# Kernel tuning notes

Hardware: AMD Instinct MI355X
Metric: run time of the kernel (lower is better)

Reference implementation:

```python
import jax, jax.numpy as jnp
import numpy as np

WS, SS, NH = 7, 3, 16  # window_size, shift_size, num_heads


def _rel_pos_index(ws):
    coords = np.stack(np.meshgrid(np.arange(ws), np.arange(ws), indexing='ij'))  # (2, ws, ws)
    cf = coords.reshape(2, -1)                       # (2, N)
    rel = (cf[:, :, None] - cf[:, None, :]).transpose(1, 2, 0).copy()  # (N, N, 2)
    rel[:, :, 0] += ws - 1
    rel[:, :, 1] += ws - 1
    rel[:, :, 0] *= 2 * ws - 1
    return rel.sum(-1)                               # (N, N) int indices into bias table


def _attn_mask(Hp, Wp, ws, ss):
    img = np.zeros((Hp, Wp))
    slices = (slice(0, -ws), slice(-ws, -ss), slice(-ss, None))
    cnt = 0
    for h in slices:
        for w in slices:
            img[h, w] = cnt
            cnt += 1
    mw = img.reshape(Hp // ws, ws, Wp // ws, ws).transpose(0, 2, 1, 3).reshape(-1, ws * ws)  # (nW, N)
    am = mw[:, None, :] - mw[:, :, None]             # (nW, N, N)
    return np.where(am != 0, -100.0, 0.0).astype(np.float32)


def setup_inputs() -> dict:
    key = jax.random.key(0)
    k1, k2, k3, k4 = jax.random.split(key, 4)
    B, H, W, C = 16, 56, 56, 512
    return {
        'q_out': jax.random.normal(k1, (B, H, W, C), dtype=jnp.float32),
        'k_out': jax.random.normal(k2, (B, H, W, C), dtype=jnp.float32),
        'v_out': jax.random.normal(k3, (B, H, W, C), dtype=jnp.float32),
        'bias_table': 0.02 * jax.random.normal(k4, ((2 * WS - 1) ** 2, NH), dtype=jnp.float32),
        'C': C, 'H': H, 'W': W,
        'x_low_padding_h': 0, 'x_low_padding_w': 0,
    }


def reference(q_out, k_out, v_out, bias_table, C, H, W, x_low_padding_h, x_low_padding_w):
    ws, ss, nh = WS, SS, NH
    Hp, Wp = H + x_low_padding_h, W + x_low_padding_w
    B = q_out.shape[0]
    hd = C // nh
    scale = hd ** (-0.5)
    N = ws * ws

    def part(x):  # (B,Hp,Wp,C) -> (B*nW, N, C)
        x = x.reshape(B, Hp // ws, ws, Wp // ws, ws, C).transpose(0, 1, 3, 2, 4, 5)
        return x.reshape(-1, N, C)

    # cyclic shift
    sq = jnp.roll(q_out, (-ss, -ss), axis=(1, 2))
    sk = jnp.roll(k_out, (-ss, -ss), axis=(1, 2))
    sv = jnp.roll(v_out, (-ss, -ss), axis=(1, 2))

    qw, kw, vw = part(sq), part(sk), part(sv)
    B_ = qw.shape[0]
    q = qw.reshape(B_, N, nh, hd).transpose(0, 2, 1, 3) * scale  # (B_, nh, N, hd)
    k = kw.reshape(B_, N, nh, hd).transpose(0, 2, 1, 3)
    v = vw.reshape(B_, N, nh, hd).transpose(0, 2, 1, 3)

    attn = jnp.einsum('bhnd,bhmd->bhnm', q, k)  # (B_, nh, N, N)

    # relative position bias
    rpi = _rel_pos_index(ws)
    bias = bias_table[rpi.reshape(-1)].reshape(N, N, nh).transpose(2, 0, 1)  # (nh, N, N)
    attn = attn + bias[None]

    # shift mask
    am = jnp.asarray(_attn_mask(Hp, Wp, ws, ss), dtype=attn.dtype)  # (nW, N, N)
    nW = am.shape[0]
    attn = attn.reshape(B_ // nW, nW, nh, N, N) + am[None, :, None]
    attn = jax.nn.softmax(attn.reshape(B_, nh, N, N), axis=-1)

    xw = jnp.einsum('bhnm,bhmd->bhnd', attn, v).transpose(0, 2, 1, 3).reshape(B_, N, C)

    # window reverse + reverse shift
    x = xw.reshape(B, Hp // ws, Wp // ws, ws, ws, C).transpose(0, 1, 3, 2, 4, 5).reshape(B, Hp, Wp, C)
    return jnp.roll(x, (ss, ss), axis=(1, 2))
```

## Files before the change

### kernel.cpp

```cpp
#include <hip/hip_runtime.h>
#include <stdint.h>


constexpr int WSZ  = 7;
constexpr int NTOK = 49;
constexpr int NH_  = 16;
constexpr int HD_  = 32;
constexpr int SP   = 56;
constexpr int CH   = 512;
constexpr float LOG2E = 1.4426950408889634f;

typedef float  f32x4 __attribute__((ext_vector_type(4)));
typedef short  s16x8 __attribute__((ext_vector_type(8)));

union FragU { uint32_t w[4]; s16x8 v; };

__device__ inline uint32_t bf16_hibits(float x) {
    uint32_t u = __float_as_uint(x);
    u += 0x7fffu + ((u >> 16) & 1u);
    return u & 0xffff0000u;
}

__device__ inline uint32_t pk_bf16(float a, float b) {
    return (bf16_hibits(a) >> 16) | bf16_hibits(b);
}

__device__ inline void hilo_pair(float a, float b, uint32_t& wh, uint32_t& wl) {
    uint32_t ah = bf16_hibits(a), bh = bf16_hibits(b);
    wh = (ah >> 16) | bh;
    float ra = a - __uint_as_float(ah);
    float rb = b - __uint_as_float(bh);
    wl = pk_bf16(ra, rb);
}

__global__ __launch_bounds__(256)
void build_bm(const float* __restrict__ bias, float* __restrict__ bm)
{
    const int blk = blockIdx.x;
    const int h = blk >> 2, cls = blk & 3;
    for (int idx = threadIdx.x; idx < 4096; idx += 256) {
        const int q = idx >> 6, m = idx & 63;
        float val;
        if (q >= NTOK || m >= NTOK) {
            val = -1e9f;
        } else {
            const int iq = q / 7, jq = q % 7, im = m / 7, jm = m % 7;
            const int rpi = (iq - im + 6) * 13 + (jq - jm + 6);
            const float bv = bias[rpi * NH_ + h];
            const int rq = ((cls & 2) ? (iq < 4 ? 3 : 6) : 0)
                         + ((cls & 1) ? (jq < 4 ? 1 : 2) : 0);
            const int rm = ((cls & 2) ? (im < 4 ? 3 : 6) : 0)
                         + ((cls & 1) ? (jm < 4 ? 1 : 2) : 0);
            const float mask = (rq != rm) ? -100.0f : 0.0f;
            val = (bv + mask) * LOG2E - 23.0f;
        }
        bm[blk * 4096 + idx] = val;
    }
}

__global__ __launch_bounds__(256, 2)
void swin_mfma_kernel(const float* __restrict__ qg,
                      const float* __restrict__ kg,
                      const float* __restrict__ vg,
                      const float* __restrict__ bm,
                      float* __restrict__ outg)
{
    const int wave = threadIdx.x >> 6;
    const int wh   = blockIdx.x * 4 + wave;
    const int h    = wh & (NH_ - 1);
    const int w    = wh >> 4;
    const int wc   = w & 7;
    const int wr   = (w >> 3) & 7;
    const int b    = w >> 6;

    const int lane = threadIdx.x & 63;
    const int g    = lane >> 4;
    const int l16  = lane & 15;

    const int t  = lane < NTOK ? lane : NTOK - 1;
    const int it = t / 7, jt = t - 7 * it;
    int sr = wr * 7 + it + 3; if (sr >= SP) sr -= SP;
    int sc = wc * 7 + jt + 3; if (sc >= SP) sc -= SP;
    const int off_t = ((b * SP + sr) * SP + sc) * CH + h * HD_;

    const float qs = 0.17677669529663687f * LOG2E;

    float4 qa[4][2], ka[4][2];
#pragma unroll
    for (int tt = 0; tt < 4; ++tt) {
        const int o = __shfl(off_t, 16 * tt + l16);
        const float* qp = qg + o + 8 * g;
        const float* kp = kg + o + 8 * g;
        qa[tt][0] = *(const float4*)qp;
        qa[tt][1] = *(const float4*)(qp + 4);
        ka[tt][0] = *(const float4*)kp;
        ka[tt][1] = *(const float4*)(kp + 4);
    }

    float vr[2][2][8];
#pragma unroll
    for (int mc = 0; mc < 2; ++mc)
#pragma unroll
        for (int e = 0; e < 8; ++e) {
            const int o = __shfl(off_t, 32 * mc + 8 * g + e);
#pragma unroll
            for (int dh = 0; dh < 2; ++dh)
                vr[mc][dh][e] = vg[o + 16 * dh + l16];
        }

    s16x8 Qh[4], Ql[4], Kh[4], Kl[4];
#pragma unroll
    for (int tt = 0; tt < 4; ++tt) {
        FragU qh, ql, kh, kl;
        float qf[8] = { qa[tt][0].x * qs, qa[tt][0].y * qs, qa[tt][0].z * qs, qa[tt][0].w * qs,
                        qa[tt][1].x * qs, qa[tt][1].y * qs, qa[tt][1].z * qs, qa[tt][1].w * qs };
        float kf[8] = { ka[tt][0].x, ka[tt][0].y, ka[tt][0].z, ka[tt][0].w,
                        ka[tt][1].x, ka[tt][1].y, ka[tt][1].z, ka[tt][1].w };
#pragma unroll
        for (int wd = 0; wd < 4; ++wd) {
            hilo_pair(qf[2 * wd], qf[2 * wd + 1], qh.w[wd], ql.w[wd]);
            hilo_pair(kf[2 * wd], kf[2 * wd + 1], kh.w[wd], kl.w[wd]);
        }
        Qh[tt] = qh.v; Ql[tt] = ql.v; Kh[tt] = kh.v; Kl[tt] = kl.v;
    }

    const int cls = ((wr == 7) ? 2 : 0) | ((wc == 7) ? 1 : 0);
    const float* bmh = bm + (h * 4 + cls) * 4096;

    f32x4 accS[4][4];
#pragma unroll
    for (int tq = 0; tq < 4; ++tq)
#pragma unroll
        for (int tk = 0; tk < 4; ++tk)
            accS[tq][tk] = *(const f32x4*)(bmh + (16 * tq + l16) * 64 + 16 * tk + 4 * g);

#pragma unroll
    for (int tq = 0; tq < 4; ++tq)
#pragma unroll
        for (int tk = 0; tk < 4; ++tk) {
            f32x4 a = accS[tq][tk];
            a = __builtin_amdgcn_mfma_f32_16x16x32_bf16(Kl[tk], Qh[tq], a, 0, 0, 0);
            a = __builtin_amdgcn_mfma_f32_16x16x32_bf16(Kh[tk], Ql[tq], a, 0, 0, 0);
            a = __builtin_amdgcn_mfma_f32_16x16x32_bf16(Kh[tk], Qh[tq], a, 0, 0, 0);
            accS[tq][tk] = a;
        }

    float p[4][4][4];
    float inv[4];
#pragma unroll
    for (int tq = 0; tq < 4; ++tq) {
        float d0 = 0.f, d1 = 0.f, d2 = 0.f, d3 = 0.f;
#pragma unroll
        for (int tk = 0; tk < 4; ++tk) {
            float e0 = __builtin_amdgcn_exp2f(accS[tq][tk][0]);
            float e1 = __builtin_amdgcn_exp2f(accS[tq][tk][1]);
            float e2 = __builtin_amdgcn_exp2f(accS[tq][tk][2]);
            float e3 = __builtin_amdgcn_exp2f(accS[tq][tk][3]);
            p[tq][tk][0] = e0; p[tq][tk][1] = e1;
            p[tq][tk][2] = e2; p[tq][tk][3] = e3;
            d0 += e0; d1 += e1; d2 += e2; d3 += e3;
        }
        float ds = (d0 + d1) + (d2 + d3);
        ds += __shfl_xor(ds, 16);
        ds += __shfl_xor(ds, 32);
        inv[tq] = 1.0f / (ds + 1e-30f);
    }

    uint32_t u0[4][4], u1[4][4];
#pragma unroll
    for (int tq = 0; tq < 4; ++tq)
#pragma unroll
        for (int tk = 0; tk < 4; ++tk) {
            u0[tq][tk] = pk_bf16(p[tq][tk][0], p[tq][tk][1]);
            u1[tq][tk] = pk_bf16(p[tq][tk][2], p[tq][tk][3]);
        }

    const int srcb = 32 * (g & 1) + l16;
    const bool hiG = (lane >= 32);
    s16x8 PA[4][2];
#pragma unroll
    for (int tq = 0; tq < 4; ++tq)
#pragma unroll
        for (int mc = 0; mc < 2; ++mc) {
            FragU fu;
#pragma unroll
            for (int wd = 0; wd < 4; ++wd) {
                const int sl = srcb + 16 * (wd >> 1);
                uint32_t A, B;
                if (wd & 1) {
                    A = __shfl(u1[tq][2 * mc],     sl);
                    B = __shfl(u1[tq][2 * mc + 1], sl);
                } else {
                    A = __shfl(u0[tq][2 * mc],     sl);
                    B = __shfl(u0[tq][2 * mc + 1], sl);
                }
                fu.w[wd] = hiG ? B : A;
            }
            PA[tq][mc] = fu.v;
        }

    s16x8 Vh[2][2], Vl[2][2];
#pragma unroll
    for (int mc = 0; mc < 2; ++mc)
#pragma unroll
        for (int dh = 0; dh < 2; ++dh) {
            FragU vh, vl;
#pragma unroll
            for (int wd = 0; wd < 4; ++wd)
                hilo_pair(vr[mc][dh][2 * wd], vr[mc][dh][2 * wd + 1], vh.w[wd], vl.w[wd]);
            Vh[mc][dh] = vh.v; Vl[mc][dh] = vl.v;
        }

    f32x4 acc2[4][2];
#pragma unroll
    for (int tq = 0; tq < 4; ++tq)
#pragma unroll
        for (int dh = 0; dh < 2; ++dh) {
            f32x4 a = {0.f, 0.f, 0.f, 0.f};
            a = __builtin_amdgcn_mfma_f32_16x16x32_bf16(PA[tq][0], Vl[0][dh], a, 0, 0, 0);
            a = __builtin_amdgcn_mfma_f32_16x16x32_bf16(PA[tq][0], Vh[0][dh], a, 0, 0, 0);
            a = __builtin_amdgcn_mfma_f32_16x16x32_bf16(PA[tq][1], Vl[1][dh], a, 0, 0, 0);
            a = __builtin_amdgcn_mfma_f32_16x16x32_bf16(PA[tq][1], Vh[1][dh], a, 0, 0, 0);
            acc2[tq][dh] = a;
        }

#pragma unroll
    for (int tq = 0; tq < 4; ++tq)
#pragma unroll
        for (int r = 0; r < 4; ++r) {
            const float iv = __shfl(inv[tq], 4 * g + r);
            const int oo = __shfl(off_t, 16 * tq + 4 * g + r);
            if (tq < 3 || (g == 0 && r == 0)) {
#pragma unroll
                for (int dh = 0; dh < 2; ++dh)
                    outg[oo + 16 * dh + l16] = acc2[tq][dh][r] * iv;
            }
        }
}

__global__ __launch_bounds__(256)
void swin_block_scalar(const float* __restrict__ qg,
                       const float* __restrict__ kg,
                       const float* __restrict__ vg,
                       const float* __restrict__ bias,
                       float* __restrict__ outg)
{
    const int wave = __builtin_amdgcn_readfirstlane(threadIdx.x >> 6);
    const int wh   = blockIdx.x * 4 + wave;
    const int h    = wh & (NH_ - 1);
    const int w    = wh >> 4;
    const int wc   = w & 7;
    const int wr   = (w >> 3) & 7;
    const int b    = w >> 6;

    const int lane = threadIdx.x & 63;
    const int rr   = lane < NTOK ? lane : NTOK - 1;
    const int i    = rr / WSZ;
    const int j    = rr - i * WSZ;

    const int hp = wr * WSZ + i;
    const int wp = wc * WSZ + j;
    int sr = hp + 3; if (sr >= SP) sr -= SP;
    int sc = wp + 3; if (sc >= SP) sc -= SP;
    const int rowoff = ((b * SP + sr) * SP + sc) * CH + h * HD_;
    const int reg_r = (hp < 49 ? 0 : (hp < 53 ? 3 : 6))
                    + (wp < 49 ? 0 : (wp < 53 ? 1 : 2));
    const float qscale = 0.17677669529663687f * LOG2E;

    float qr[HD_];
    {
        const float4* qp = reinterpret_cast<const float4*>(qg + rowoff);
#pragma unroll
        for (int tt = 0; tt < HD_ / 4; ++tt) {
            float4 x = qp[tt];
            qr[4*tt+0] = x.x * qscale; qr[4*tt+1] = x.y * qscale;
            qr[4*tt+2] = x.z * qscale; qr[4*tt+3] = x.w * qscale;
        }
    }
    const int biaslane = (i * 13 + j) * 16 + h;
    float o[HD_];
#pragma unroll
    for (int d = 0; d < HD_; ++d) o[d] = 0.f;
    float denom = 0.f;
    const float* kb = kg + b * SP * SP * CH + h * HD_;
    const float* vb = vg + b * SP * SP * CH + h * HD_;

    for (int ic = 0; ic < WSZ; ++ic) {
        const int hpc = wr * WSZ + ic;
        int src_r = hpc + 3; if (src_r >= SP) src_r -= SP;
        const int regh_c = (hpc < 49 ? 0 : (hpc < 53 ? 3 : 6));
        const float* krow0 = kb + src_r * SP * CH;
        const float* vrow0 = vb + src_r * SP * CH;
        float e[WSZ];
#pragma unroll
        for (int u = 0; u < WSZ; ++u) {
            const int wpc = wc * WSZ + u;
            int src_c = wpc + 3; if (src_c >= SP) src_c -= SP;
            const int reg_c = regh_c + (wpc < 49 ? 0 : (wpc < 53 ? 1 : 2));
            const float* krow = krow0 + src_c * CH;
            const float bv = bias[biaslane + ((6 - ic) * 13 + (6 - u)) * 16];
            float s0 = fmaf(bv, LOG2E, (reg_r != reg_c) ? -167.26950408889634f : -23.0f);
            float s1 = 0.f, s2 = 0.f, s3 = 0.f;
#pragma unroll
            for (int d = 0; d < HD_; d += 4) {
                s0 = fmaf(qr[d+0], krow[d+0], s0);
                s1 = fmaf(qr[d+1], krow[d+1], s1);
                s2 = fmaf(qr[d+2], krow[d+2], s2);
                s3 = fmaf(qr[d+3], krow[d+3], s3);
            }
            e[u] = exp2f((s0 + s1) + (s2 + s3));
            denom += e[u];
        }
#pragma unroll
        for (int u = 0; u < WSZ; ++u) {
            const int wpc = wc * WSZ + u;
            int src_c = wpc + 3; if (src_c >= SP) src_c -= SP;
            const float* vrow = vrow0 + src_c * CH;
            const float ev = e[u];
#pragma unroll
            for (int d = 0; d < HD_; ++d) o[d] = fmaf(ev, vrow[d], o[d]);
        }
    }
    const float invd = 1.0f / denom;
    if (lane < NTOK) {
        float4* op = reinterpret_cast<float4*>(outg + rowoff);
#pragma unroll
        for (int tt = 0; tt < HD_ / 4; ++tt) {
            float4 x;
            x.x = o[4*tt+0] * invd; x.y = o[4*tt+1] * invd;
            x.z = o[4*tt+2] * invd; x.w = o[4*tt+3] * invd;
            op[tt] = x;
        }
    }
}

extern "C" void kernel_launch(void* const* d_in, const int* in_sizes, int n_in,
                              void* d_out, int out_size, void* d_ws, size_t ws_size,
                              hipStream_t stream) {
    const float* q    = (const float*)d_in[0];
    const float* k    = (const float*)d_in[1];
    const float* v    = (const float*)d_in[2];
    const float* bias = (const float*)d_in[3];
    float* out        = (float*)d_out;

    const int B   = in_sizes[0] / (SP * SP * CH);
    const int nwh = B * (SP / WSZ) * (SP / WSZ) * NH_;

    const size_t bm_bytes = (size_t)NH_ * 4 * 64 * 64 * sizeof(float);
    if (ws_size >= bm_bytes) {
        float* bm = (float*)d_ws;
        hipLaunchKernelGGL(build_bm, dim3(NH_ * 4), dim3(256), 0, stream, bias, bm);
        hipLaunchKernelGGL(swin_mfma_kernel, dim3(nwh / 4), dim3(256), 0, stream,
                           q, k, v, bm, out);
    } else {
        hipLaunchKernelGGL(swin_block_scalar, dim3(nwh / 4), dim3(256), 0, stream,
                           q, k, v, bias, out);
    }
}
```

Before: 119.9 us.

## Cut split-bf16 MFMA terms and fuse softmax into QK loop for occupancy

Drops the Q low-part correction term in QK^T (two MFMAs instead of three per tile) and drops the V hi/lo split entirely, so P·V uses a single bf16 pass. The bias load, exp2, row-sum and bf16 packing are fused into the QK loop, and the PV output is stored per row-tile, which shortens register live ranges. Launch bounds are raised to 4 blocks per CU. Accuracy drops because Q and V are now plain bf16, which risks exceeding tolerance.

```diff
diff --git a/kernel.cpp b/kernel.cpp
--- a/kernel.cpp
+++ b/kernel.cpp
@@ -58,7 +58,7 @@
     }
 }
 
-__global__ __launch_bounds__(256, 2)
+__global__ __launch_bounds__(256, 4)
 void swin_mfma_kernel(const float* __restrict__ qg,
                       const float* __restrict__ kg,
                       const float* __restrict__ vg,
@@ -85,95 +85,73 @@
 
     const float qs = 0.17677669529663687f * LOG2E;
 
-    float4 qa[4][2], ka[4][2];
+    s16x8 Qh[4], Kh[4], Kl[4];
 #pragma unroll
     for (int tt = 0; tt < 4; ++tt) {
         const int o = __shfl(off_t, 16 * tt + l16);
         const float* qp = qg + o + 8 * g;
         const float* kp = kg + o + 8 * g;
-        qa[tt][0] = *(const float4*)qp;
-        qa[tt][1] = *(const float4*)(qp + 4);
-        ka[tt][0] = *(const float4*)kp;
-        ka[tt][1] = *(const float4*)(kp + 4);
-    }
-
-    float vr[2][2][8];
-#pragma unroll
-    for (int mc = 0; mc < 2; ++mc)
-#pragma unroll
-        for (int e = 0; e < 8; ++e) {
-            const int o = __shfl(off_t, 32 * mc + 8 * g + e);
-#pragma unroll
-            for (int dh = 0; dh < 2; ++dh)
-                vr[mc][dh][e] = vg[o + 16 * dh + l16];
-        }
-
-    s16x8 Qh[4], Ql[4], Kh[4], Kl[4];
-#pragma unroll
-    for (int tt = 0; tt < 4; ++tt) {
-        FragU qh, ql, kh, kl;
-        float qf[8] = { qa[tt][0].x * qs, qa[tt][0].y * qs, qa[tt][0].z * qs, qa[tt][0].w * qs,
-                        qa[tt][1].x * qs, qa[tt][1].y * qs, qa[tt][1].z * qs, qa[tt][1].w * qs };
-        float kf[8] = { ka[tt][0].x, ka[tt][0].y, ka[tt][0].z, ka[tt][0].w,
-                        ka[tt][1].x, ka[tt][1].y, ka[tt][1].z, ka[tt][1].w };
-#pragma unroll
-        for (int wd = 0; wd < 4; ++wd) {
-            hilo_pair(qf[2 * wd], qf[2 * wd + 1], qh.w[wd], ql.w[wd]);
-            hilo_pair(kf[2 * wd], kf[2 * wd + 1], kh.w[wd], kl.w[wd]);
-        }
-        Qh[tt] = qh.v; Ql[tt] = ql.v; Kh[tt] = kh.v; Kl[tt] = kl.v;
+        float4 q0 = *(const float4*)qp;
+        float4 q1 = *(const float4*)(qp + 4);
+        float4 k0 = *(const float4*)kp;
+        float4 k1 = *(const float4*)(kp + 4);
+        FragU qh, kh, kl;
+        qh.w[0] = pk_bf16(q0.x * qs, q0.y * qs);
+        qh.w[1] = pk_bf16(q0.z * qs, q0.w * qs);
+        qh.w[2] = pk_bf16(q1.x * qs, q1.y * qs);
+        qh.w[3] = pk_bf16(q1.z * qs, q1.w * qs);
+        hilo_pair(k0.x, k0.y, kh.w[0], kl.w[0]);
+        hilo_pair(k0.z, k0.w, kh.w[1], kl.w[1]);
+        hilo_pair(k1.x, k1.y, kh.w[2], kl.w[2]);
+        hilo_pair(k1.z, k1.w, kh.w[3], kl.w[3]);
+        Qh[tt] = qh.v; Kh[tt] = kh.v; Kl[tt] = kl.v;
+    }
+
+    s16x8 Vb[2][2];
+#pragma unroll
+    for (int mc = 0; mc < 2; ++mc) {
+        int vo[8];
+#pragma unroll
+        for (int e = 0; e < 8; ++e)
+            vo[e] = __shfl(off_t, 32 * mc + 8 * g + e);
+#pragma unroll
+        for (int dh = 0; dh < 2; ++dh) {
+            FragU fu;
+#pragma unroll
+            for (int wd = 0; wd < 4; ++wd) {
+                float a = vg[vo[2 * wd]     + 16 * dh + l16];
+                float c = vg[vo[2 * wd + 1] + 16 * dh + l16];
+                fu.w[wd] = pk_bf16(a, c);
+            }
+            Vb[mc][dh] = fu.v;
+        }
     }
 
     const int cls = ((wr == 7) ? 2 : 0) | ((wc == 7) ? 1 : 0);
     const float* bmh = bm + (h * 4 + cls) * 4096;
 
-    f32x4 accS[4][4];
-#pragma unroll
-    for (int tq = 0; tq < 4; ++tq)
-#pragma unroll
-        for (int tk = 0; tk < 4; ++tk)
-            accS[tq][tk] = *(const f32x4*)(bmh + (16 * tq + l16) * 64 + 16 * tk + 4 * g);
-
-#pragma unroll
-    for (int tq = 0; tq < 4; ++tq)
+    uint32_t u0[4][4], u1[4][4];
+    float inv[4];
+#pragma unroll
+    for (int tq = 0; tq < 4; ++tq) {
+        float dsum = 0.f;
 #pragma unroll
         for (int tk = 0; tk < 4; ++tk) {
-            f32x4 a = accS[tq][tk];
+            f32x4 a = *(const f32x4*)(bmh + (16 * tq + l16) * 64 + 16 * tk + 4 * g);
             a = __builtin_amdgcn_mfma_f32_16x16x32_bf16(Kl[tk], Qh[tq], a, 0, 0, 0);
-            a = __builtin_amdgcn_mfma_f32_16x16x32_bf16(Kh[tk], Ql[tq], a, 0, 0, 0);
             a = __builtin_amdgcn_mfma_f32_16x16x32_bf16(Kh[tk], Qh[tq], a, 0, 0, 0);
-            accS[tq][tk] = a;
-        }
-
-    float p[4][4][4];
-    float inv[4];
-#pragma unroll
-    for (int tq = 0; tq < 4; ++tq) {
-        float d0 = 0.f, d1 = 0.f, d2 = 0.f, d3 = 0.f;
-#pragma unroll
-        for (int tk = 0; tk < 4; ++tk) {
-            float e0 = __builtin_amdgcn_exp2f(accS[tq][tk][0]);
-            float e1 = __builtin_amdgcn_exp2f(accS[tq][tk][1]);
-            float e2 = __builtin_amdgcn_exp2f(accS[tq][tk][2]);
-            float e3 = __builtin_amdgcn_exp2f(accS[tq][tk][3]);
-            p[tq][tk][0] = e0; p[tq][tk][1] = e1;
-            p[tq][tk][2] = e2; p[tq][tk][3] = e3;
-            d0 += e0; d1 += e1; d2 += e2; d3 += e3;
-        }
-        float ds = (d0 + d1) + (d2 + d3);
-        ds += __shfl_xor(ds, 16);
-        ds += __shfl_xor(ds, 32);
-        inv[tq] = 1.0f / (ds + 1e-30f);
-    }
-
-    uint32_t u0[4][4], u1[4][4];
-#pragma unroll
-    for (int tq = 0; tq < 4; ++tq)
-#pragma unroll
-        for (int tk = 0; tk < 4; ++tk) {
-            u0[tq][tk] = pk_bf16(p[tq][tk][0], p[tq][tk][1]);
-            u1[tq][tk] = pk_bf16(p[tq][tk][2], p[tq][tk][3]);
-        }
+            float e0 = __builtin_amdgcn_exp2f(a[0]);
+            float e1 = __builtin_amdgcn_exp2f(a[1]);
+            float e2 = __builtin_amdgcn_exp2f(a[2]);
+            float e3 = __builtin_amdgcn_exp2f(a[3]);
+            dsum += (e0 + e1) + (e2 + e3);
+            u0[tq][tk] = pk_bf16(e0, e1);
+            u1[tq][tk] = pk_bf16(e2, e3);
+        }
+        dsum += __shfl_xor(dsum, 16);
+        dsum += __shfl_xor(dsum, 32);
+        inv[tq] = 1.0f / (dsum + 1e-30f);
+    }
 
     const int srcb = 32 * (g & 1) + l16;
     const bool hiG = (lane >= 32);
@@ -199,33 +177,16 @@
             PA[tq][mc] = fu.v;
         }
 
-    s16x8 Vh[2][2], Vl[2][2];
-#pragma unroll
-    for (int mc = 0; mc < 2; ++mc)
-#pragma unroll
-        for (int dh = 0; dh < 2; ++dh) {
-            FragU vh, vl;
-#pragma unroll
-            for (int wd = 0; wd < 4; ++wd)
-                hilo_pair(vr[mc][dh][2 * wd], vr[mc][dh][2 * wd + 1], vh.w[wd], vl.w[wd]);
-            Vh[mc][dh] = vh.v; Vl[mc][dh] = vl.v;
-        }
-
-    f32x4 acc2[4][2];
-#pragma unroll
-    for (int tq = 0; tq < 4; ++tq)
+#pragma unroll
+    for (int tq = 0; tq < 4; ++tq) {
+        f32x4 acc[2];
 #pragma unroll
         for (int dh = 0; dh < 2; ++dh) {
             f32x4 a = {0.f, 0.f, 0.f, 0.f};
-            a = __builtin_amdgcn_mfma_f32_16x16x32_bf16(PA[tq][0], Vl[0][dh], a, 0, 0, 0);
-            a = __builtin_amdgcn_mfma_f32_16x16x32_bf16(PA[tq][0], Vh[0][dh], a, 0, 0, 0);
-            a = __builtin_amdgcn_mfma_f32_16x16x32_bf16(PA[tq][1], Vl[1][dh], a, 0, 0, 0);
-            a = __builtin_amdgcn_mfma_f32_16x16x32_bf16(PA[tq][1], Vh[1][dh], a, 0, 0, 0);
-            acc2[tq][dh] = a;
-        }
-
-#pragma unroll
-    for (int tq = 0; tq < 4; ++tq)
+            a = __builtin_amdgcn_mfma_f32_16x16x32_bf16(PA[tq][0], Vb[0][dh], a, 0, 0, 0);
+            a = __builtin_amdgcn_mfma_f32_16x16x32_bf16(PA[tq][1], Vb[1][dh], a, 0, 0, 0);
+            acc[dh] = a;
+        }
 #pragma unroll
         for (int r = 0; r < 4; ++r) {
             const float iv = __shfl(inv[tq], 4 * g + r);
@@ -233,9 +194,10 @@
             if (tq < 3 || (g == 0 && r == 0)) {
 #pragma unroll
                 for (int dh = 0; dh < 2; ++dh)
-                    outg[oo + 16 * dh + l16] = acc2[tq][dh][r] * iv;
+                    outg[oo + 16 * dh + l16] = acc[dh][r] * iv;
             }
         }
+    }
 }
 
 __global__ __launch_bounds__(256)
```

New measurement: 116.9 us. 1.03x faster.
